# Kernel tuning notes

Measured on AMD Instinct MI355X. Metric: run time of the kernel, lower is better.

Reference implementation:

```python
import jax, jax.numpy as jnp
import numpy as np

N = 50000      # nodes
E = 800000     # edges (avg degree 16)
IN = 128       # in_size
OUT = 64       # out_size
H = 32         # hidden_size
WIDTH = 3      # width
SCALE = 0.05


def _laplacian(x, src, tgt, n):
    # normalized Laplacian action: out[t] = sum_{edges into t} (x[t] - x[s]) / deg(t)
    deg = jax.ops.segment_sum(jnp.ones((tgt.shape[0],), x.dtype), tgt, num_segments=n)
    fac = 1.0 / deg[tgt]                       # [E], deg>=1 for any target that appears
    msg = (x[tgt] - x[src]) * fac[:, None]     # [E, F]
    return jax.ops.segment_sum(msg, tgt, num_segments=n)


def _grouped_linear(x, Wg, bg):
    # Conv1d(kernel=1, groups=width) == per-group linear
    n = x.shape[0]
    xg = x.reshape(n, WIDTH, -1)               # [N, width, h_in]
    out = jnp.einsum('nwh,who->nwo', xg, Wg) + bg
    return out.reshape(n, -1)                  # [N, width*h_out]


def setup_inputs() -> dict:
    key = jax.random.key(0)
    ks = jax.random.split(key, 14)
    data = jax.random.normal(ks[0], (N, IN), jnp.float32)
    src = jax.random.randint(ks[1], (E,), 0, N)
    tgt = jnp.sort(jax.random.randint(ks[2], (E,), 0, N))
    # preprocess ConvSkip: Linear(in, hidden*width) + Linear(in, hidden*width)
    W_pre = jax.random.normal(ks[3], (IN, H * WIDTH), jnp.float32) * SCALE
    b_pre = jnp.zeros((H * WIDTH,), jnp.float32)
    T_pre = jax.random.normal(ks[4], (IN, H * WIDTH), jnp.float32) * SCALE
    bT_pre = jnp.zeros((H * WIDTH,), jnp.float32)
    # middle WideConvSkip (depth-2 = 1 block): grouped conv [width, H, H]
    W_blk = jax.random.normal(ks[5], (WIDTH, H, H), jnp.float32) * SCALE
    b_blk = jnp.zeros((WIDTH, H), jnp.float32)
    T_blk = jax.random.normal(ks[6], (IN, H * WIDTH), jnp.float32) * SCALE
    bT_blk = jnp.zeros((H * WIDTH,), jnp.float32)
    # postprocess WideConvSkip: grouped conv [width, H, OUT]
    W_post = jax.random.normal(ks[7], (WIDTH, H, OUT), jnp.float32) * SCALE
    b_post = jnp.zeros((WIDTH, OUT), jnp.float32)
    T_post = jax.random.normal(ks[8], (IN, OUT * WIDTH), jnp.float32) * SCALE
    bT_post = jnp.zeros((OUT * WIDTH,), jnp.float32)
    return {"data": data, "src": src, "tgt": tgt,
            "W_pre": W_pre, "b_pre": b_pre, "T_pre": T_pre, "bT_pre": bT_pre,
            "W_blk": W_blk, "b_blk": b_blk, "T_blk": T_blk, "bT_blk": bT_blk,
            "W_post": W_post, "b_post": b_post, "T_post": T_post, "bT_post": bT_post}


def reference(data, src, tgt, W_pre, b_pre, T_pre, bT_pre,
              W_blk, b_blk, T_blk, bT_blk,
              W_post, b_post, T_post, bT_post):
    n = data.shape[0]
    # preprocess ConvSkip: sigma(L f(x) + g(x))
    out = data @ W_pre + b_pre
    out = _laplacian(out, src, tgt, n)
    out = jax.nn.relu(out + data @ T_pre + bT_pre)       # [N, H*width]
    # middle WideConvSkip (depth - 2 = 1)
    h = _grouped_linear(out, W_blk, b_blk)
    h = _laplacian(h, src, tgt, n)
    out = jax.nn.relu(h + data @ T_blk + bT_blk)          # [N, H*width]
    # postprocess WideConvSkip
    h = _grouped_linear(out, W_post, b_post)
    h = _laplacian(h, src, tgt, n)
    out = jax.nn.relu(h + data @ T_post + bT_post)        # [N, OUT*width]
    # reshape(N, -1, width) then adaptive_avg_pool1d(., 1) == mean over width
    out = out.reshape(n, -1, WIDTH)
    return out.mean(axis=-1, keepdims=True)               # [N, OUT, 1]
```

## Files before the change

kernel.cpp:

```cpp
#include <hip/hip_runtime.h>
#include <cstdint>
#include <cstddef>

#define N_NODES 50000
#define E_EDGES 800000
#define IN_F    128
#define PCOLS   512

typedef unsigned short ushortT;
typedef unsigned int   uintT;
typedef __attribute__((ext_vector_type(8))) short s8v;
typedef __attribute__((ext_vector_type(4))) float f4v;
typedef __attribute__((ext_vector_type(2))) float f2v;

__device__ __forceinline__ float bflo(uintT u){ union{uintT i;float f;}c; c.i=u<<16; return c.f; }
__device__ __forceinline__ float bfhi(uintT u){ union{uintT i;float f;}c; c.i=u&0xFFFF0000u; return c.f; }
__device__ __forceinline__ ushortT f2bfu(float f){
    union{float f;uintT u;}c; c.f=f;
    uintT r = c.u + 0x7FFF + ((c.u>>16)&1);
    return (ushortT)(r>>16);
}
__device__ __forceinline__ uintT pack2(float a, float b){
    return (uintT)f2bfu(a) | ((uintT)f2bfu(b) << 16);
}

__global__ void prep1(const float* __restrict__ A,
                      const float* __restrict__ Wp,  const float* __restrict__ bp,
                      const float* __restrict__ Tp,  const float* __restrict__ bTp,
                      const float* __restrict__ Tb,  const float* __restrict__ bTb,
                      const float* __restrict__ Tpo, const float* __restrict__ bTpo,
                      const float* __restrict__ Wpost,
                      const int* __restrict__ tgt,
                      ushortT* __restrict__ Wb, float* __restrict__ bcat,
                      float2* __restrict__ Wp2,
                      ushortT* __restrict__ Ab, int* __restrict__ row_ptr,
                      ushortT* __restrict__ Pb, ushortT* __restrict__ rb1,
                      ushortT* __restrict__ rb2)
{
    int gid = blockIdx.x * 256 + threadIdx.x;
    {
        size_t off = (size_t)gid * 8;
        float4 v0 = *(const float4*)(A + off);
        float4 v1 = *(const float4*)(A + off + 4);
        uint4 u;
        u.x = pack2(v0.x, v0.y); u.y = pack2(v0.z, v0.w);
        u.z = pack2(v1.x, v1.y); u.w = pack2(v1.z, v1.w);
        *(uint4*)(Ab + off) = u;
    }
    if (gid < IN_F * PCOLS) {
        int k = gid >> 9;
        int c = gid & 511;
        float v;
        if      (c < 96)  v = Wp [k*96  + c];
        else if (c < 192) v = Tp [k*96  + (c-96)];
        else if (c < 288) v = Tb [k*96  + (c-192)];
        else if (c < 480) v = Tpo[k*192 + (c-288)];
        else              v = 0.f;
        Wb[(size_t)c*IN_F + k] = f2bfu(v);
        if (k == 0) {
            float b;
            if      (c < 96)  b = bp  [c];
            else if (c < 192) b = bTp [c-96];
            else if (c < 288) b = bTb [c-192];
            else if (c < 480) b = bTpo[c-288];
            else              b = 0.f;
            bcat[c] = b;
        }
        if (gid < 3*16*64) {
            int w = gid >> 10, r = gid & 1023;
            int i2 = r >> 6, j = r & 63;
            Wp2[gid] = make_float2(Wpost[(w*32 + 2*i2)*64 + j],
                                   Wpost[(w*32 + 2*i2 + 1)*64 + j]);
        }
    }
    if (gid < 96) {
        Pb [(size_t)N_NODES*PCOLS + gid] = 0;
        rb1[(size_t)N_NODES*96   + gid] = 0;
        rb2[(size_t)N_NODES*96   + gid] = 0;
    }
    if (gid <= N_NODES) {
        int lo = 0, hi = E_EDGES;
        while (lo < hi) {
            int mid = (lo + hi) >> 1;
            if (tgt[mid] < gid) lo = mid + 1; else hi = mid;
        }
        row_ptr[gid] = lo;
    }
}

__global__ __launch_bounds__(256, 4) void gemm_mfma(const ushortT* __restrict__ Ab,
                                                    const ushortT* __restrict__ Wb,
                                                    const float* __restrict__ bcat,
                                                    ushortT* __restrict__ Pb, int M)
{
    __shared__ ushortT Bsl[128][136];
    int tid = threadIdx.x;
    int i = blockIdx.x;
    int xcd = i & 7, j = i >> 3;
    int nb = (j & 3) * 128;
    int mb = (xcd * 49 + (j >> 2)) * 128;
    int wv = tid >> 6, lane = tid & 63;
    int wm = wv >> 1, wn = wv & 1;
    int cl = lane & 15, q = lane >> 4;

    #pragma unroll
    for (int r = 0; r < 8; ++r) {
        int idx = tid + 256*r;
        int row = idx >> 4, qq = idx & 15;
        uint4 v = *(const uint4*)(Wb + (size_t)(nb+row)*IN_F + qq*8);
        *(uint4*)(&Bsl[row][qq*8]) = v;
    }
    __syncthreads();

    f4v acc[4][4];
    #pragma unroll
    for (int a = 0; a < 4; ++a)
        #pragma unroll
        for (int b = 0; b < 4; ++b) acc[a][b] = (f4v)0.f;

    int gmBase = mb + wm*64;
    #pragma unroll
    for (int ks = 0; ks < 4; ++ks) {
        int ko = ks*32 + q*8;
        s8v af[4], bf[4];
        #pragma unroll
        for (int mt = 0; mt < 4; ++mt) {
            int gm = gmBase + mt*16 + cl;
            uint4 va = make_uint4(0,0,0,0);
            if (gm < M) va = *(const uint4*)(Ab + (size_t)gm*IN_F + ko);
            af[mt] = *(s8v*)&va;
        }
        #pragma unroll
        for (int nt = 0; nt < 4; ++nt)
            bf[nt] = *(const s8v*)(&Bsl[wn*64 + nt*16 + cl][ko]);
        #pragma unroll
        for (int mt = 0; mt < 4; ++mt)
            #pragma unroll
            for (int nt = 0; nt < 4; ++nt)
                acc[mt][nt] = __builtin_amdgcn_mfma_f32_16x16x32_bf16(af[mt], bf[nt], acc[mt][nt], 0, 0, 0);
    }

    __syncthreads();

    #pragma unroll
    for (int nt = 0; nt < 4; ++nt) {
        int cn = wn*64 + nt*16 + cl;
        float bv = bcat[nb + cn];
        #pragma unroll
        for (int mt = 0; mt < 4; ++mt) {
            int rm0 = wm*64 + mt*16 + q*4;
            #pragma unroll
            for (int r = 0; r < 4; ++r)
                Bsl[rm0 + r][cn] = f2bfu(acc[mt][nt][r] + bv);
        }
    }
    __syncthreads();

    #pragma unroll
    for (int p = 0; p < 8; ++p) {
        int idx = tid + 256*p;
        int row = idx >> 4, sg = idx & 15;
        int gm = mb + row;
        if (gm < M) {
            uint4 v = *(const uint4*)(&Bsl[row][sg*8]);
            *(uint4*)(Pb + (size_t)gm*PCOLS + nb + sg*8) = v;
        }
    }
}

#define ISSUE_W(Xb, sv, pL, w_, u)                                                \
    _Pragma("unroll")                                                             \
    for (int kk = 0; kk < 16; ++kk) {                                             \
        int off = __builtin_amdgcn_readlane(sv, (w_) + kk);                       \
        u[kk] = *(const uintT*)((const char*)(Xb) + off + 4*(pL));                \
    }

#define SUM_W(u, c0, c1, c2, c3)                                                  \
    _Pragma("unroll")                                                             \
    for (int kk = 0; kk < 16; ++kk) {                                             \
        f2v v_; v_.x = bflo(u[kk]); v_.y = bfhi(u[kk]);                           \
        switch (kk & 3) {                                                         \
            case 0: c0 += v_; break;                                              \
            case 1: c1 += v_; break;                                              \
            case 2: c2 += v_; break;                                              \
            default:c3 += v_; break;                                              \
        }                                                                         \
    }

#define GATHER_REST(Xb, lo, deg, sv, pL, STRB, u, c0, c1, c2, c3)                 \
    {                                                                             \
        int dmax_ = (deg) < 64 ? (deg) : 64;                                      \
        _Pragma("unroll 1")                                                       \
        for (int w_ = 16; w_ < dmax_; w_ += 16) {                                 \
            ISSUE_W(Xb, sv, pL, w_, u)                                            \
            SUM_W(u, c0, c1, c2, c3)                                              \
        }                                                                         \
        if ((deg) > 64) {                                                         \
            _Pragma("unroll 1")                                                   \
            for (int j_ = (lo) + 64; j_ < (lo) + (deg); ++j_) {                   \
                int off = src[j_] * (STRB);                                       \
                uintT u0 = *(const uintT*)((const char*)(Xb) + off + 4*(pL));     \
                f2v v_; v_.x = bflo(u0); v_.y = bfhi(u0);                         \
                c0 += v_;                                                         \
            }                                                                     \
        }                                                                         \
    }

#define MAKE_SV(lo, deg, lane, STRB, sv)                                          \
    int sv;                                                                       \
    {                                                                             \
        int e_ = (lo) + (lane);                                                   \
        if (e_ > E_EDGES - 1) e_ = E_EDGES - 1;                                   \
        int sn_ = src[e_];                                                        \
        sv = ((lane) < (deg) ? sn_ : N_NODES) * (STRB);                           \
    }

__global__ __launch_bounds__(256) void lap1(
    const ushortT* __restrict__ Pb,
    const int* __restrict__ src, const int* __restrict__ row_ptr,
    ushortT* __restrict__ rb1)
{
    int lane = threadIdx.x & 63;
    int tA = __builtin_amdgcn_readfirstlane(blockIdx.x*8 + (threadIdx.x >> 6)*2);
    int tB = tA + 1;
    int loA = __builtin_amdgcn_readfirstlane(row_ptr[tA]);
    int degA = __builtin_amdgcn_readfirstlane(row_ptr[tA+1]) - loA;
    int loB = __builtin_amdgcn_readfirstlane(row_ptr[tB]);
    int degB = __builtin_amdgcn_readfirstlane(row_ptr[tB+1]) - loB;
    int pL = lane < 48 ? lane : 0;
    MAKE_SV(loA, degA, lane, 2*PCOLS, svA)
    MAKE_SV(loB, degB, lane, 2*PCOLS, svB)
    uintT uxA = *(const uintT*)(Pb + (size_t)tA*PCOLS + 2*pL);
    uintT zuA = *(const uintT*)(Pb + (size_t)tA*PCOLS + 96 + 2*pL);
    uintT uxB = *(const uintT*)(Pb + (size_t)tB*PCOLS + 2*pL);
    uintT zuB = *(const uintT*)(Pb + (size_t)tB*PCOLS + 96 + 2*pL);

    uintT uA[16], uB[16];
    ISSUE_W(Pb, svA, pL, 0, uA)
    ISSUE_W(Pb, svB, pL, 0, uB)

    {
        f2v c0={0.f,0.f}, c1={0.f,0.f}, c2={0.f,0.f}, c3={0.f,0.f};
        SUM_W(uA, c0, c1, c2, c3)
        GATHER_REST(Pb, loA, degA, svA, pL, 2*PCOLS, uA, c0, c1, c2, c3)
        f2v cs = (c0 + c1) + (c2 + c3);
        float inv = degA > 0 ? 1.f/(float)degA : 0.f;
        float mf  = degA > 0 ? 1.f : 0.f;
        if (lane < 48) {
            float ox = fmaxf(mf*bflo(uxA) - cs.x*inv + bflo(zuA), 0.f);
            float oy = fmaxf(mf*bfhi(uxA) - cs.y*inv + bfhi(zuA), 0.f);
            *(uintT*)(rb1 + (size_t)tA*96 + 2*pL) = pack2(ox, oy);
        }
    }
    {
        f2v c0={0.f,0.f}, c1={0.f,0.f}, c2={0.f,0.f}, c3={0.f,0.f};
        SUM_W(uB, c0, c1, c2, c3)
        GATHER_REST(Pb, loB, degB, svB, pL, 2*PCOLS, uB, c0, c1, c2, c3)
        f2v cs = (c0 + c1) + (c2 + c3);
        float inv = degB > 0 ? 1.f/(float)degB : 0.f;
        float mf  = degB > 0 ? 1.f : 0.f;
        if (lane < 48) {
            float ox = fmaxf(mf*bflo(uxB) - cs.x*inv + bflo(zuB), 0.f);
            float oy = fmaxf(mf*bfhi(uxB) - cs.y*inv + bfhi(zuB), 0.f);
            *(uintT*)(rb1 + (size_t)tB*96 + 2*pL) = pack2(ox, oy);
        }
    }
}

__global__ __launch_bounds__(256) void lap2(
    const ushortT* __restrict__ Xb,
    const ushortT* __restrict__ Pb,
    const int* __restrict__ src, const int* __restrict__ row_ptr,
    const float* __restrict__ Wblk,
    ushortT* __restrict__ rb2)
{
    __shared__ float wS[3*32*32];
    for (int i = threadIdx.x; i < 3072; i += 256) wS[i] = Wblk[i];
    __syncthreads();

    int lane = threadIdx.x & 63;
    int wvw  = threadIdx.x >> 6;
    int pL = lane < 48 ? lane : 0;
    int w  = pL >> 4;
    int jj = pL & 15;
    const float2* wc = ((const float2*)wS) + (w*512 + jj);

#define LAP2_NODE(t, lo, deg, sv, ux, zu, u)                                      \
    {                                                                             \
        f2v c0={0.f,0.f}, c1={0.f,0.f}, c2={0.f,0.f}, c3={0.f,0.f};               \
        SUM_W(u, c0, c1, c2, c3)                                                  \
        GATHER_REST(Xb, lo, deg, sv, pL, 192, u, c0, c1, c2, c3)                  \
        f2v cs = (c0 + c1) + (c2 + c3);                                           \
        float inv = (deg) > 0 ? 1.f/(float)(deg) : 0.f;                           \
        float mf  = (deg) > 0 ? 1.f : 0.f;                                        \
        float Lx = mf*bflo(ux) - cs.x*inv;                                        \
        float Ly = mf*bfhi(ux) - cs.y*inv;                                        \
        float accx = 0.f, accy = 0.f;                                             \
        _Pragma("unroll")                                                         \
        for (int d = 0; d < 16; ++d) {                                            \
            int sl = w*16 + d;                                                    \
            float ax = __shfl(Lx, sl);                                            \
            float ay = __shfl(Ly, sl);                                            \
            float2 wa = wc[(2*d)*16];                                             \
            float2 wb = wc[(2*d+1)*16];                                           \
            accx = fmaf(ax, wa.x, accx); accx = fmaf(ay, wb.x, accx);             \
            accy = fmaf(ax, wa.y, accy); accy = fmaf(ay, wb.y, accy);             \
        }                                                                         \
        if (lane < 48) {                                                          \
            float ox = fmaxf(accx + bflo(zu), 0.f);                               \
            float oy = fmaxf(accy + bfhi(zu), 0.f);                               \
            *(uintT*)(rb2 + (size_t)(t)*96 + 2*pL) = pack2(ox, oy);               \
        }                                                                         \
    }

    #pragma unroll 1
    for (int it = 0; it < 2; ++it) {
        int tA = __builtin_amdgcn_readfirstlane(blockIdx.x*16 + it*8 + wvw*2);
        int tB = tA + 1;
        int loA = __builtin_amdgcn_readfirstlane(row_ptr[tA]);
        int degA = __builtin_amdgcn_readfirstlane(row_ptr[tA+1]) - loA;
        int loB = __builtin_amdgcn_readfirstlane(row_ptr[tB]);
        int degB = __builtin_amdgcn_readfirstlane(row_ptr[tB+1]) - loB;
        MAKE_SV(loA, degA, lane, 192, svA)
        MAKE_SV(loB, degB, lane, 192, svB)
        uintT uxA = *(const uintT*)(Xb + (size_t)tA*96 + 2*pL);
        uintT zuA = *(const uintT*)(Pb + (size_t)tA*PCOLS + 192 + 2*pL);
        uintT uxB = *(const uintT*)(Xb + (size_t)tB*96 + 2*pL);
        uintT zuB = *(const uintT*)(Pb + (size_t)tB*PCOLS + 192 + 2*pL);

        uintT uA[16], uB[16];
        ISSUE_W(Xb, svA, pL, 0, uA)
        ISSUE_W(Xb, svB, pL, 0, uB)

        LAP2_NODE(tA, loA, degA, svA, uxA, zuA, uA)
        LAP2_NODE(tB, loB, degB, svB, uxB, zuB, uB)
    }
#undef LAP2_NODE
}

__global__ __launch_bounds__(256) void lap3(
    const ushortT* __restrict__ Xb,
    const ushortT* __restrict__ Pb,
    const int* __restrict__ src, const int* __restrict__ row_ptr,
    const float2* __restrict__ Wp2,
    float* __restrict__ out)
{
    __shared__ float2 wS[3*16*64];
    __shared__ float  sm[4][96];
    for (int i = threadIdx.x; i < 3072; i += 256) wS[i] = Wp2[i];
    __syncthreads();

    int lane = threadIdx.x & 63;
    int wvw  = threadIdx.x >> 6;
    int pL = lane < 48 ? lane : 0;
    const float2* wl = wS + lane;

#define LAP3_NODE(t, lo, deg, sv, ux, z0, z1, z2, u)                              \
    {                                                                             \
        f2v c0={0.f,0.f}, c1={0.f,0.f}, c2={0.f,0.f}, c3={0.f,0.f};               \
        SUM_W(u, c0, c1, c2, c3)                                                  \
        GATHER_REST(Xb, lo, deg, sv, pL, 192, u, c0, c1, c2, c3)                  \
        f2v cs = (c0 + c1) + (c2 + c3);                                           \
        float inv = (deg) > 0 ? 1.f/(float)(deg) : 0.f;                           \
        float mf  = (deg) > 0 ? 1.f : 0.f;                                        \
        float Lx = mf*bflo(ux) - cs.x*inv;                                        \
        float Ly = mf*bfhi(ux) - cs.y*inv;                                        \
        if (lane < 48) {                                                          \
            sm[wvw][2*pL]     = Lx;                                               \
            sm[wvw][2*pL + 1] = Ly;                                               \
        }                                                                         \
        __builtin_amdgcn_wave_barrier();                                          \
        float a0 = 0.f, a1 = 0.f, a2 = 0.f;                                       \
        _Pragma("unroll")                                                         \
        for (int w2 = 0; w2 < 3; ++w2) {                                          \
            float acc = 0.f;                                                      \
            _Pragma("unroll")                                                     \
            for (int i2 = 0; i2 < 16; ++i2) {                                     \
                float2 iv = *(const float2*)(&sm[wvw][w2*32 + 2*i2]);             \
                float2 p  = wl[(w2*16 + i2)*64];                                  \
                acc = fmaf(iv.x, p.x, acc);                                       \
                acc = fmaf(iv.y, p.y, acc);                                       \
            }                                                                     \
            if (w2 == 0) a0 = acc; else if (w2 == 1) a1 = acc; else a2 = acc;     \
        }                                                                         \
        __builtin_amdgcn_wave_barrier();                                          \
        float o0 = fmaxf(a0 + z0, 0.f);                                           \
        float o1 = fmaxf(a1 + z1, 0.f);                                           \
        float o2 = fmaxf(a2 + z2, 0.f);                                           \
        float r = 0.f;                                                            \
        _Pragma("unroll")                                                         \
        for (int q = 0; q < 3; ++q) {                                             \
            int c = 3*lane + q;                                                   \
            int sl = c & 63, wsel = c >> 6;                                       \
            float v0 = __shfl(o0, sl);                                            \
            float v1 = __shfl(o1, sl);                                            \
            float v2 = __shfl(o2, sl);                                            \
            r += (wsel == 0) ? v0 : ((wsel == 1) ? v1 : v2);                      \
        }                                                                         \
        out[(size_t)(t)*64 + lane] = r * (1.0f/3.0f);                             \
    }

    #pragma unroll 1
    for (int it = 0; it < 2; ++it) {
        int tA = __builtin_amdgcn_readfirstlane(blockIdx.x*16 + it*8 + wvw*2);
        int tB = tA + 1;
        int loA = __builtin_amdgcn_readfirstlane(row_ptr[tA]);
        int degA = __builtin_amdgcn_readfirstlane(row_ptr[tA+1]) - loA;
        int loB = __builtin_amdgcn_readfirstlane(row_ptr[tB]);
        int degB = __builtin_amdgcn_readfirstlane(row_ptr[tB+1]) - loB;
        MAKE_SV(loA, degA, lane, 192, svA)
        MAKE_SV(loB, degB, lane, 192, svB)
        uintT uxA = *(const uintT*)(Xb + (size_t)tA*96 + 2*pL);
        float z0A = bflo((uintT)Pb[(size_t)tA*PCOLS + 288 + lane]);
        float z1A = bflo((uintT)Pb[(size_t)tA*PCOLS + 352 + lane]);
        float z2A = bflo((uintT)Pb[(size_t)tA*PCOLS + 416 + lane]);
        uintT uxB = *(const uintT*)(Xb + (size_t)tB*96 + 2*pL);
        float z0B = bflo((uintT)Pb[(size_t)tB*PCOLS + 288 + lane]);
        float z1B = bflo((uintT)Pb[(size_t)tB*PCOLS + 352 + lane]);
        float z2B = bflo((uintT)Pb[(size_t)tB*PCOLS + 416 + lane]);

        uintT uA[16], uB[16];
        ISSUE_W(Xb, svA, pL, 0, uA)
        ISSUE_W(Xb, svB, pL, 0, uB)

        LAP3_NODE(tA, loA, degA, svA, uxA, z0A, z1A, z2A, uA)
        LAP3_NODE(tB, loB, degB, svB, uxB, z0B, z1B, z2B, uB)
    }
#undef LAP3_NODE
}

extern "C" void kernel_launch(void* const* d_in, const int* in_sizes, int n_in,
                              void* d_out, int out_size, void* d_ws, size_t ws_size,
                              hipStream_t stream)
{
    const float* data    = (const float*)d_in[0];
    const int*   src     = (const int*)  d_in[1];
    const int*   tgt     = (const int*)  d_in[2];
    const float* W_pre   = (const float*)d_in[3];
    const float* b_pre   = (const float*)d_in[4];
    const float* T_pre   = (const float*)d_in[5];
    const float* bT_pre  = (const float*)d_in[6];
    const float* W_blk   = (const float*)d_in[7];
    const float* b_blk   = (const float*)d_in[8];
    const float* T_blk   = (const float*)d_in[9];
    const float* bT_blk  = (const float*)d_in[10];
    const float* W_post  = (const float*)d_in[11];
    const float* b_post  = (const float*)d_in[12];
    const float* T_post  = (const float*)d_in[13];
    const float* bT_post = (const float*)d_in[14];
    float* out = (float*)d_out;

    float*   ws      = (float*)d_ws;
    float*   bcat    = ws;
    float2*  Wp2     = (float2*)(bcat + 512);
    int*     row_ptr = (int*)(Wp2 + 3*16*64);
    ushortT* Pb      = (ushortT*)(row_ptr + 50008);
    ushortT* rb1     = Pb  + (size_t)(N_NODES+1) * PCOLS;
    ushortT* rb2     = rb1 + (size_t)(N_NODES+1) * 96;
    ushortT* Ab      = rb2 + (size_t)(N_NODES+1) * 96;
    ushortT* Wb      = Ab  + (size_t)N_NODES * IN_F;

    prep1<<<(N_NODES*IN_F/8)/256, 256, 0, stream>>>(
        data, W_pre, b_pre, T_pre, bT_pre, T_blk, bT_blk, T_post, bT_post,
        W_post, tgt, Wb, bcat, Wp2, Ab, row_ptr, Pb, rb1, rb2);

    gemm_mfma<<<1568, 256, 0, stream>>>(Ab, Wb, bcat, Pb, N_NODES);

    lap1<<<N_NODES/8, 256, 0, stream>>>(Pb, src, row_ptr, rb1);
    lap2<<<N_NODES/16, 256, 0, stream>>>(rb1, Pb, src, row_ptr, W_blk, rb2);
    lap3<<<N_NODES/16, 256, 0, stream>>>(rb2, Pb, src, row_ptr, Wp2, out);
}
```

Measured before the change: 283.6 us.

## Gather neighbor features in FP8 with packed lane layout for Laplacian kernels

Adds FP8 (e4m3) shadow copies of the per-node feature buffers (a new conversion kernel for the first stage, dual bf16+fp8 stores in lap1/lap2). The neighbor gathers read 4-byte fp8 quads, with lanes split into two halves that each process alternate edges via ds_bpermute, and then reduce with shuffles. This cuts the bytes fetched per random gather. Each wave now handles 4 nodes with all descriptors loaded up front. It risks accuracy loss from fp8 quantization and adds an extra launch plus extra stores.

```diff
diff --git a/kernel.cpp b/kernel.cpp
--- a/kernel.cpp
+++ b/kernel.cpp
@@ -1,4 +1,5 @@
 #include <hip/hip_runtime.h>
+#include <hip/hip_fp8.h>
 #include <cstdint>
 #include <cstddef>
 
@@ -9,6 +10,7 @@
 
 typedef unsigned short ushortT;
 typedef unsigned int   uintT;
+typedef unsigned char  u8T;
 typedef __attribute__((ext_vector_type(8))) short s8v;
 typedef __attribute__((ext_vector_type(4))) float f4v;
 typedef __attribute__((ext_vector_type(2))) float f2v;
@@ -23,6 +25,25 @@
 __device__ __forceinline__ uintT pack2(float a, float b){
     return (uintT)f2bfu(a) | ((uintT)f2bfu(b) << 16);
 }
+__device__ __forceinline__ float f8f(uintT b){
+    __hip_fp8_e4m3 h; h.__x = (__hip_fp8_storage_t)(b & 0xFF); return (float)h;
+}
+__device__ __forceinline__ uintT ff8(float f){
+    __hip_fp8_e4m3 h(f); return (uintT)h.__x;
+}
+__device__ __forceinline__ f2v cvtpk_sw(uintT u, bool hi){
+    uintT w = hi ? (u >> 16) : u;
+    f2v r; r.x = f8f(w); r.y = f8f(w >> 8); return r;
+}
+#if defined(__has_builtin)
+#if __has_builtin(__builtin_amdgcn_cvt_pk_f32_fp8)
+#define CVTPK(u, hi) __builtin_amdgcn_cvt_pk_f32_fp8((u), (hi))
+#else
+#define CVTPK(u, hi) cvtpk_sw((u), (hi))
+#endif
+#else
+#define CVTPK(u, hi) cvtpk_sw((u), (hi))
+#endif
 
 __global__ void prep1(const float* __restrict__ A,
                       const float* __restrict__ Wp,  const float* __restrict__ bp,
@@ -34,8 +55,7 @@
                       ushortT* __restrict__ Wb, float* __restrict__ bcat,
                       float2* __restrict__ Wp2,
                       ushortT* __restrict__ Ab, int* __restrict__ row_ptr,
-                      ushortT* __restrict__ Pb, ushortT* __restrict__ rb1,
-                      ushortT* __restrict__ rb2)
+                      u8T* __restrict__ rb1f8, u8T* __restrict__ rb2f8)
 {
     int gid = blockIdx.x * 256 + threadIdx.x;
     {
@@ -73,10 +93,9 @@
                                    Wpost[(w*32 + 2*i2 + 1)*64 + j]);
         }
     }
-    if (gid < 96) {
-        Pb [(size_t)N_NODES*PCOLS + gid] = 0;
-        rb1[(size_t)N_NODES*96   + gid] = 0;
-        rb2[(size_t)N_NODES*96   + gid] = 0;
+    if (gid < 24) {
+        *(uintT*)(rb1f8 + (size_t)N_NODES*96 + 4*gid) = 0;
+        *(uintT*)(rb2f8 + (size_t)N_NODES*96 + 4*gid) = 0;
     }
     if (gid <= N_NODES) {
         int lo = 0, hi = E_EDGES;
@@ -168,133 +187,166 @@
     }
 }
 
-#define ISSUE_W(Xb, sv, pL, w_, u)                                                \
+__global__ void cvt_y0(const ushortT* __restrict__ Pb, u8T* __restrict__ Y8)
+{
+    int gid = blockIdx.x * 256 + threadIdx.x;
+    if (gid < N_NODES*24) {
+        int t = gid / 24, q = gid - t*24;
+        uint2 rv = *(const uint2*)(Pb + (size_t)t*PCOLS + 4*q);
+        uintT o = ff8(bflo(rv.x)) | (ff8(bfhi(rv.x)) << 8)
+                | (ff8(bflo(rv.y)) << 16) | (ff8(bfhi(rv.y)) << 24);
+        *(uintT*)(Y8 + (size_t)t*96 + 4*q) = o;
+    } else if (gid < N_NODES*24 + 24) {
+        *(uintT*)(Y8 + (size_t)N_NODES*96 + 4*(gid - N_NODES*24)) = 0;
+    }
+}
+
+#define LANE_GEO8                                                                 \
+    int lane = threadIdx.x & 63;                                                  \
+    int pL = lane < 48 ? lane : 0;                                                \
+    int lq = (lane < 24) ? lane : ((lane < 48) ? lane - 24 : lane - 48);          \
+    int bpb = (lane >= 24 && lane < 48) ? 4 : 0;          \
+    int in4 = 4*lq;
+
+#define GPK_W(X8, sv, S0, CNT, u)                                                 \
     _Pragma("unroll")                                                             \
-    for (int kk = 0; kk < 16; ++kk) {                                             \
-        int off = __builtin_amdgcn_readlane(sv, (w_) + kk);                       \
-        u[kk] = *(const uintT*)((const char*)(Xb) + off + 4*(pL));                \
-    }
-
-#define SUM_W(u, c0, c1, c2, c3)                                                  \
+    for (int s_ = 0; s_ < (CNT); ++s_) {                                          \
+        int vr_ = __builtin_amdgcn_ds_bpermute(bpb + 8*((S0)+s_), sv);            \
+        u[s_] = *(const uintT*)((const u8T*)(X8) + (uintT)(vr_ + in4));           \
+    }
+#define GPK_D(u, CNT, a0, a1, b0, b1)                                             \
     _Pragma("unroll")                                                             \
-    for (int kk = 0; kk < 16; ++kk) {                                             \
-        f2v v_; v_.x = bflo(u[kk]); v_.y = bfhi(u[kk]);                           \
-        switch (kk & 3) {                                                         \
-            case 0: c0 += v_; break;                                              \
-            case 1: c1 += v_; break;                                              \
-            case 2: c2 += v_; break;                                              \
-            default:c3 += v_; break;                                              \
-        }                                                                         \
-    }
-
-#define GATHER_REST(Xb, lo, deg, sv, pL, STRB, u, c0, c1, c2, c3)                 \
+    for (int s_ = 0; s_ < (CNT); ++s_) {                                          \
+        f2v l_ = CVTPK(u[s_], 0);                                                 \
+        f2v h_ = CVTPK(u[s_], 1);                                                 \
+        if (s_ & 1) { b0 += l_; b1 += h_; } else { a0 += l_; a1 += h_; }          \
+    }
+#define GATHER_PK(X8, lo, deg, sv, sx, sy)                                        \
+    float sx, sy;                                                                 \
     {                                                                             \
-        int dmax_ = (deg) < 64 ? (deg) : 64;                                      \
-        _Pragma("unroll 1")                                                       \
-        for (int w_ = 16; w_ < dmax_; w_ += 16) {                                 \
-            ISSUE_W(Xb, sv, pL, w_, u)                                            \
-            SUM_W(u, c0, c1, c2, c3)                                              \
-        }                                                                         \
-        if ((deg) > 64) {                                                         \
+        f2v a0={0.f,0.f}, a1={0.f,0.f}, b0={0.f,0.f}, b1={0.f,0.f};               \
+        uintT u[12];                                                              \
+        GPK_W(X8, sv, 0, 12, u)                                                   \
+        GPK_D(u, 12, a0, a1, b0, b1)                                              \
+        if (deg > 24) {                                                           \
+            GPK_W(X8, sv, 12, 12, u)                                              \
+            GPK_D(u, 12, a0, a1, b0, b1)                                          \
+        }                                                                         \
+        if (deg > 48) {                                                           \
+            GPK_W(X8, sv, 24, 8, u)                                               \
+            GPK_D(u, 8, a0, a1, b0, b1)                                           \
+        }                                                                         \
+        if (deg > 64) {                                                           \
             _Pragma("unroll 1")                                                   \
-            for (int j_ = (lo) + 64; j_ < (lo) + (deg); ++j_) {                   \
-                int off = src[j_] * (STRB);                                       \
-                uintT u0 = *(const uintT*)((const char*)(Xb) + off + 4*(pL));     \
-                f2v v_; v_.x = bflo(u0); v_.y = bfhi(u0);                         \
-                c0 += v_;                                                         \
+            for (int j_ = lo + 64; j_ < lo + deg; ++j_) {                         \
+                int off_ = src[j_] * 96;                                          \
+                uintT t_ = *(const uintT*)((const u8T*)(X8) + (uintT)(off_ + in4));\
+                if (lane < 24) { a0 += CVTPK(t_, 0); a1 += CVTPK(t_, 1); }        \
             }                                                                     \
         }                                                                         \
-    }
-
-#define MAKE_SV(lo, deg, lane, STRB, sv)                                          \
-    int sv;                                                                       \
+        f2v va = a0 + b0, vb = a1 + b1;        \
+         \
+        int pl_ = (lane < 24) ? lane + 24 : ((lane < 48) ? lane - 24 : lane);     \
+        va.x += __shfl(va.x, pl_); va.y += __shfl(va.y, pl_);                     \
+        vb.x += __shfl(vb.x, pl_); vb.y += __shfl(vb.y, pl_);                     \
+        int fl_ = pL >> 1;                                                        \
+        float e0_ = __shfl(va.x, fl_), e1_ = __shfl(va.y, fl_);                   \
+        float e2_ = __shfl(vb.x, fl_), e3_ = __shfl(vb.y, fl_);                   \
+        sx = (pL & 1) ? e2_ : e0_;                                                \
+        sy = (pL & 1) ? e3_ : e1_;                                                \
+    }
+
+#define DESC4(t0)                                                                 \
+    int lo0,dg0,sv0, lo1,dg1,sv1, lo2,dg2,sv2, lo3,dg3,sv3;                       \
     {                                                                             \
-        int e_ = (lo) + (lane);                                                   \
-        if (e_ > E_EDGES - 1) e_ = E_EDGES - 1;                                   \
-        int sn_ = src[e_];                                                        \
-        sv = ((lane) < (deg) ? sn_ : N_NODES) * (STRB);                           \
+        int rA0 = row_ptr[(t0)];    int rB0 = row_ptr[(t0)+1];                    \
+        int rA1 = row_ptr[(t0)+4];  int rB1 = row_ptr[(t0)+5];                    \
+        int rA2 = row_ptr[(t0)+8];  int rB2 = row_ptr[(t0)+9];                    \
+        int rA3 = row_ptr[(t0)+12]; int rB3 = row_ptr[(t0)+13];                   \
+        lo0 = __builtin_amdgcn_readfirstlane(rA0);                                \
+        dg0 = __builtin_amdgcn_readfirstlane(rB0) - lo0;                          \
+        lo1 = __builtin_amdgcn_readfirstlane(rA1);                                \
+        dg1 = __builtin_amdgcn_readfirstlane(rB1) - lo1;                          \
+        lo2 = __builtin_amdgcn_readfirstlane(rA2);                                \
+        dg2 = __builtin_amdgcn_readfirstlane(rB2) - lo2;                          \
+        lo3 = __builtin_amdgcn_readfirstlane(rA3);                                \
+        dg3 = __builtin_amdgcn_readfirstlane(rB3) - lo3;                          \
+        int e0 = lo0 + lane; if (e0 > E_EDGES-1) e0 = E_EDGES-1;                  \
+        int e1 = lo1 + lane; if (e1 > E_EDGES-1) e1 = E_EDGES-1;                  \
+        int e2 = lo2 + lane; if (e2 > E_EDGES-1) e2 = E_EDGES-1;                  \
+        int e3 = lo3 + lane; if (e3 > E_EDGES-1) e3 = E_EDGES-1;                  \
+        int sn0 = src[e0]; int sn1 = src[e1];                                     \
+        int sn2 = src[e2]; int sn3 = src[e3];                                     \
+        sv0 = (lane < dg0 ? sn0 : N_NODES) * 96;                                  \
+        sv1 = (lane < dg1 ? sn1 : N_NODES) * 96;                                  \
+        sv2 = (lane < dg2 ? sn2 : N_NODES) * 96;                                  \
+        sv3 = (lane < dg3 ? sn3 : N_NODES) * 96;                                  \
     }
 
 __global__ __launch_bounds__(256) void lap1(
     const ushortT* __restrict__ Pb,
+    const u8T*     __restrict__ Y8,
     const int* __restrict__ src, const int* __restrict__ row_ptr,
-    ushortT* __restrict__ rb1)
-{
-    int lane = threadIdx.x & 63;
-    int tA = __builtin_amdgcn_readfirstlane(blockIdx.x*8 + (threadIdx.x >> 6)*2);
-    int tB = tA + 1;
-    int loA = __builtin_amdgcn_readfirstlane(row_ptr[tA]);
-    int degA = __builtin_amdgcn_readfirstlane(row_ptr[tA+1]) - loA;
-    int loB = __builtin_amdgcn_readfirstlane(row_ptr[tB]);
-    int degB = __builtin_amdgcn_readfirstlane(row_ptr[tB+1]) - loB;
-    int pL = lane < 48 ? lane : 0;
-    MAKE_SV(loA, degA, lane, 2*PCOLS, svA)
-    MAKE_SV(loB, degB, lane, 2*PCOLS, svB)
-    uintT uxA = *(const uintT*)(Pb + (size_t)tA*PCOLS + 2*pL);
-    uintT zuA = *(const uintT*)(Pb + (size_t)tA*PCOLS + 96 + 2*pL);
-    uintT uxB = *(const uintT*)(Pb + (size_t)tB*PCOLS + 2*pL);
-    uintT zuB = *(const uintT*)(Pb + (size_t)tB*PCOLS + 96 + 2*pL);
-
-    uintT uA[16], uB[16];
-    ISSUE_W(Pb, svA, pL, 0, uA)
-    ISSUE_W(Pb, svB, pL, 0, uB)
-
-    {
-        f2v c0={0.f,0.f}, c1={0.f,0.f}, c2={0.f,0.f}, c3={0.f,0.f};
-        SUM_W(uA, c0, c1, c2, c3)
-        GATHER_REST(Pb, loA, degA, svA, pL, 2*PCOLS, uA, c0, c1, c2, c3)
-        f2v cs = (c0 + c1) + (c2 + c3);
-        float inv = degA > 0 ? 1.f/(float)degA : 0.f;
-        float mf  = degA > 0 ? 1.f : 0.f;
-        if (lane < 48) {
-            float ox = fmaxf(mf*bflo(uxA) - cs.x*inv + bflo(zuA), 0.f);
-            float oy = fmaxf(mf*bfhi(uxA) - cs.y*inv + bfhi(zuA), 0.f);
-            *(uintT*)(rb1 + (size_t)tA*96 + 2*pL) = pack2(ox, oy);
-        }
-    }
-    {
-        f2v c0={0.f,0.f}, c1={0.f,0.f}, c2={0.f,0.f}, c3={0.f,0.f};
-        SUM_W(uB, c0, c1, c2, c3)
-        GATHER_REST(Pb, loB, degB, svB, pL, 2*PCOLS, uB, c0, c1, c2, c3)
-        f2v cs = (c0 + c1) + (c2 + c3);
-        float inv = degB > 0 ? 1.f/(float)degB : 0.f;
-        float mf  = degB > 0 ? 1.f : 0.f;
-        if (lane < 48) {
-            float ox = fmaxf(mf*bflo(uxB) - cs.x*inv + bflo(zuB), 0.f);
-            float oy = fmaxf(mf*bfhi(uxB) - cs.y*inv + bfhi(zuB), 0.f);
-            *(uintT*)(rb1 + (size_t)tB*96 + 2*pL) = pack2(ox, oy);
-        }
-    }
+    ushortT* __restrict__ rb1, u8T* __restrict__ rb1f8)
+{
+    LANE_GEO8
+    int wvw = threadIdx.x >> 6;
+    int t0 = blockIdx.x*16 + wvw;
+    DESC4(t0)
+
+#define LAP1_IT(tt, lo, deg, sv)                                                  \
+    {                                                                             \
+        int t_ = __builtin_amdgcn_readfirstlane(tt);                              \
+        uintT ux = *(const uintT*)(Pb + (size_t)t_*PCOLS + 2*pL);                 \
+        uintT zu = *(const uintT*)(Pb + (size_t)t_*PCOLS + 96 + 2*pL);            \
+        GATHER_PK(Y8, lo, deg, sv, sx, sy)                                        \
+        float inv = (deg) > 0 ? 1.f/(float)(deg) : 0.f;                           \
+        float mf  = (deg) > 0 ? 1.f : 0.f;                                        \
+        if (lane < 48) {                                                          \
+            float ox = fmaxf(mf*bflo(ux) - sx*inv + bflo(zu), 0.f);               \
+            float oy = fmaxf(mf*bfhi(ux) - sy*inv + bfhi(zu), 0.f);               \
+            *(uintT*)(rb1 + (size_t)t_*96 + 2*pL) = pack2(ox, oy);                \
+            *(ushortT*)(rb1f8 + (size_t)t_*96 + 2*pL) =                           \
+                (ushortT)(ff8(ox) | (ff8(oy) << 8));                              \
+        }                                                                         \
+    }
+    LAP1_IT(t0,      lo0, dg0, sv0)
+    LAP1_IT(t0 + 4,  lo1, dg1, sv1)
+    LAP1_IT(t0 + 8,  lo2, dg2, sv2)
+    LAP1_IT(t0 + 12, lo3, dg3, sv3)
+#undef LAP1_IT
 }
 
 __global__ __launch_bounds__(256) void lap2(
     const ushortT* __restrict__ Xb,
+    const u8T*     __restrict__ X8,
     const ushortT* __restrict__ Pb,
     const int* __restrict__ src, const int* __restrict__ row_ptr,
     const float* __restrict__ Wblk,
-    ushortT* __restrict__ rb2)
+    ushortT* __restrict__ rb2, u8T* __restrict__ rb2f8)
 {
     __shared__ float wS[3*32*32];
     for (int i = threadIdx.x; i < 3072; i += 256) wS[i] = Wblk[i];
     __syncthreads();
 
-    int lane = threadIdx.x & 63;
-    int wvw  = threadIdx.x >> 6;
-    int pL = lane < 48 ? lane : 0;
+    LANE_GEO8
+    int wvw = threadIdx.x >> 6;
     int w  = pL >> 4;
     int jj = pL & 15;
     const float2* wc = ((const float2*)wS) + (w*512 + jj);
-
-#define LAP2_NODE(t, lo, deg, sv, ux, zu, u)                                      \
+    int t0 = blockIdx.x*16 + wvw;
+    DESC4(t0)
+
+#define LAP2_IT(tt, lo, deg, sv)                                                  \
     {                                                                             \
-        f2v c0={0.f,0.f}, c1={0.f,0.f}, c2={0.f,0.f}, c3={0.f,0.f};               \
-        SUM_W(u, c0, c1, c2, c3)                                                  \
-        GATHER_REST(Xb, lo, deg, sv, pL, 192, u, c0, c1, c2, c3)                  \
-        f2v cs = (c0 + c1) + (c2 + c3);                                           \
+        int t_ = __builtin_amdgcn_readfirstlane(tt);                              \
+        uintT ux = *(const uintT*)(Xb + (size_t)t_*96 + 2*pL);                    \
+        uintT zu = *(const uintT*)(Pb + (size_t)t_*PCOLS + 192 + 2*pL);           \
+        GATHER_PK(X8, lo, deg, sv, sx, sy)                                        \
         float inv = (deg) > 0 ? 1.f/(float)(deg) : 0.f;                           \
         float mf  = (deg) > 0 ? 1.f : 0.f;                                        \
-        float Lx = mf*bflo(ux) - cs.x*inv;                                        \
-        float Ly = mf*bfhi(ux) - cs.y*inv;                                        \
+        float Lx = mf*bflo(ux) - sx*inv;                                          \
+        float Ly = mf*bfhi(ux) - sy*inv;                                          \
         float accx = 0.f, accy = 0.f;                                             \
         _Pragma("unroll")                                                         \
         for (int d = 0; d < 16; ++d) {                                            \
@@ -309,37 +361,21 @@
         if (lane < 48) {                                                          \
             float ox = fmaxf(accx + bflo(zu), 0.f);                               \
             float oy = fmaxf(accy + bfhi(zu), 0.f);                               \
-            *(uintT*)(rb2 + (size_t)(t)*96 + 2*pL) = pack2(ox, oy);               \
-        }                                                                         \
-    }
-
-    #pragma unroll 1
-    for (int it = 0; it < 2; ++it) {
-        int tA = __builtin_amdgcn_readfirstlane(blockIdx.x*16 + it*8 + wvw*2);
-        int tB = tA + 1;
-        int loA = __builtin_amdgcn_readfirstlane(row_ptr[tA]);
-        int degA = __builtin_amdgcn_readfirstlane(row_ptr[tA+1]) - loA;
-        int loB = __builtin_amdgcn_readfirstlane(row_ptr[tB]);
-        int degB = __builtin_amdgcn_readfirstlane(row_ptr[tB+1]) - loB;
-        MAKE_SV(loA, degA, lane, 192, svA)
-        MAKE_SV(loB, degB, lane, 192, svB)
-        uintT uxA = *(const uintT*)(Xb + (size_t)tA*96 + 2*pL);
-        uintT zuA = *(const uintT*)(Pb + (size_t)tA*PCOLS + 192 + 2*pL);
-        uintT uxB = *(const uintT*)(Xb + (size_t)tB*96 + 2*pL);
-        uintT zuB = *(const uintT*)(Pb + (size_t)tB*PCOLS + 192 + 2*pL);
-
-        uintT uA[16], uB[16];
-        ISSUE_W(Xb, svA, pL, 0, uA)
-        ISSUE_W(Xb, svB, pL, 0, uB)
-
-        LAP2_NODE(tA, loA, degA, svA, uxA, zuA, uA)
-        LAP2_NODE(tB, loB, degB, svB, uxB, zuB, uB)
-    }
-#undef LAP2_NODE
+            *(uintT*)(rb2 + (size_t)t_*96 + 2*pL) = pack2(ox, oy);                \
+            *(ushortT*)(rb2f8 + (size_t)t_*96 + 2*pL) =                           \
+                (ushortT)(ff8(ox) | (ff8(oy) << 8));                              \
+        }                                                                         \
+    }
+    LAP2_IT(t0,      lo0, dg0, sv0)
+    LAP2_IT(t0 + 4,  lo1, dg1, sv1)
+    LAP2_IT(t0 + 8,  lo2, dg2, sv2)
+    LAP2_IT(t0 + 12, lo3, dg3, sv3)
+#undef LAP2_IT
 }
 
 __global__ __launch_bounds__(256) void lap3(
     const ushortT* __restrict__ Xb,
+    const u8T*     __restrict__ X8,
     const ushortT* __restrict__ Pb,
     const int* __restrict__ src, const int* __restrict__ row_ptr,
     const float2* __restrict__ Wp2,
@@ -350,21 +386,24 @@
     for (int i = threadIdx.x; i < 3072; i += 256) wS[i] = Wp2[i];
     __syncthreads();
 
-    int lane = threadIdx.x & 63;
-    int wvw  = threadIdx.x >> 6;
-    int pL = lane < 48 ? lane : 0;
+    LANE_GEO8
+    int wvw = threadIdx.x >> 6;
     const float2* wl = wS + lane;
-
-#define LAP3_NODE(t, lo, deg, sv, ux, z0, z1, z2, u)                              \
+    int t0 = blockIdx.x*16 + wvw;
+    DESC4(t0)
+
+#define LAP3_IT(tt, lo, deg, sv)                                                  \
     {                                                                             \
-        f2v c0={0.f,0.f}, c1={0.f,0.f}, c2={0.f,0.f}, c3={0.f,0.f};               \
-        SUM_W(u, c0, c1, c2, c3)                                                  \
-        GATHER_REST(Xb, lo, deg, sv, pL, 192, u, c0, c1, c2, c3)                  \
-        f2v cs = (c0 + c1) + (c2 + c3);                                           \
+        int t_ = __builtin_amdgcn_readfirstlane(tt);                              \
+        uintT ux = *(const uintT*)(Xb + (size_t)t_*96 + 2*pL);                    \
+        float z0 = bflo((uintT)Pb[(size_t)t_*PCOLS + 288 + lane]);                \
+        float z1 = bflo((uintT)Pb[(size_t)t_*PCOLS + 352 + lane]);                \
+        float z2 = bflo((uintT)Pb[(size_t)t_*PCOLS + 416 + lane]);                \
+        GATHER_PK(X8, lo, deg, sv, sx, sy)                                        \
         float inv = (deg) > 0 ? 1.f/(float)(deg) : 0.f;                           \
         float mf  = (deg) > 0 ? 1.f : 0.f;                                        \
-        float Lx = mf*bflo(ux) - cs.x*inv;                                        \
-        float Ly = mf*bfhi(ux) - cs.y*inv;                                        \
+        float Lx = mf*bflo(ux) - sx*inv;                                          \
+        float Ly = mf*bfhi(ux) - sy*inv;                                          \
         if (lane < 48) {                                                          \
             sm[wvw][2*pL]     = Lx;                                               \
             sm[wvw][2*pL + 1] = Ly;                                               \
@@ -397,36 +436,13 @@
             float v2 = __shfl(o2, sl);                                            \
             r += (wsel == 0) ? v0 : ((wsel == 1) ? v1 : v2);                      \
         }                                                                         \
-        out[(size_t)(t)*64 + lane] = r * (1.0f/3.0f);                             \
-    }
-
-    #pragma unroll 1
-    for (int it = 0; it < 2; ++it) {
-        int tA = __builtin_amdgcn_readfirstlane(blockIdx.x*16 + it*8 + wvw*2);
-        int tB = tA + 1;
-        int loA = __builtin_amdgcn_readfirstlane(row_ptr[tA]);
-        int degA = __builtin_amdgcn_readfirstlane(row_ptr[tA+1]) - loA;
-        int loB = __builtin_amdgcn_readfirstlane(row_ptr[tB]);
-        int degB = __builtin_amdgcn_readfirstlane(row_ptr[tB+1]) - loB;
-        MAKE_SV(loA, degA, lane, 192, svA)
-        MAKE_SV(loB, degB, lane, 192, svB)
-        uintT uxA = *(const uintT*)(Xb + (size_t)tA*96 + 2*pL);
-        float z0A = bflo((uintT)Pb[(size_t)tA*PCOLS + 288 + lane]);
-        float z1A = bflo((uintT)Pb[(size_t)tA*PCOLS + 352 + lane]);
-        float z2A = bflo((uintT)Pb[(size_t)tA*PCOLS + 416 + lane]);
-        uintT uxB = *(const uintT*)(Xb + (size_t)tB*96 + 2*pL);
-        float z0B = bflo((uintT)Pb[(size_t)tB*PCOLS + 288 + lane]);
-        float z1B = bflo((uintT)Pb[(size_t)tB*PCOLS + 352 + lane]);
-        float z2B = bflo((uintT)Pb[(size_t)tB*PCOLS + 416 + lane]);
-
-        uintT uA[16], uB[16];
-        ISSUE_W(Xb, svA, pL, 0, uA)
-        ISSUE_W(Xb, svB, pL, 0, uB)
-
-        LAP3_NODE(tA, loA, degA, svA, uxA, z0A, z1A, z2A, uA)
-        LAP3_NODE(tB, loB, degB, svB, uxB, z0B, z1B, z2B, uB)
-    }
-#undef LAP3_NODE
+        out[(size_t)t_*64 + lane] = r * (1.0f/3.0f);                              \
+    }
+    LAP3_IT(t0,      lo0, dg0, sv0)
+    LAP3_IT(t0 + 4,  lo1, dg1, sv1)
+    LAP3_IT(t0 + 8,  lo2, dg2, sv2)
+    LAP3_IT(t0 + 12, lo3, dg3, sv3)
+#undef LAP3_IT
 }
 
 extern "C" void kernel_launch(void* const* d_in, const int* in_sizes, int n_in,
@@ -459,14 +475,19 @@
     ushortT* rb2     = rb1 + (size_t)(N_NODES+1) * 96;
     ushortT* Ab      = rb2 + (size_t)(N_NODES+1) * 96;
     ushortT* Wb      = Ab  + (size_t)N_NODES * IN_F;
+    u8T*     Y8      = (u8T*)(Wb + 512*IN_F);
+    u8T*     rb1f8   = Y8  + (size_t)(N_NODES+1) * 96;
+    u8T*     rb2f8   = rb1f8 + (size_t)(N_NODES+1) * 96;
 
     prep1<<<(N_NODES*IN_F/8)/256, 256, 0, stream>>>(
         data, W_pre, b_pre, T_pre, bT_pre, T_blk, bT_blk, T_post, bT_post,
-        W_post, tgt, Wb, bcat, Wp2, Ab, row_ptr, Pb, rb1, rb2);
+        W_post, tgt, Wb, bcat, Wp2, Ab, row_ptr, rb1f8, rb2f8);
 
     gemm_mfma<<<1568, 256, 0, stream>>>(Ab, Wb, bcat, Pb, N_NODES);
 
-    lap1<<<N_NODES/8, 256, 0, stream>>>(Pb, src, row_ptr, rb1);
-    lap2<<<N_NODES/16, 256, 0, stream>>>(rb1, Pb, src, row_ptr, W_blk, rb2);
-    lap3<<<N_NODES/16, 256, 0, stream>>>(rb2, Pb, src, row_ptr, Wp2, out);
-}
+    cvt_y0<<<(N_NODES*24 + 24 + 255)/256, 256, 0, stream>>>(Pb, Y8);
+
+    lap1<<<N_NODES/16, 256, 0, stream>>>(Pb, Y8, src, row_ptr, rb1, rb1f8);
+    lap2<<<N_NODES/16, 256, 0, stream>>>(rb1, rb1f8, Pb, src, row_ptr, W_blk, rb2, rb2f8);
+    lap3<<<N_NODES/16, 256, 0, stream>>>(rb2, rb2f8, Pb, src, row_ptr, Wp2, out);
+}
```

Result: faster. 269.2 us (-5.1%).
